# Optimization experiments

Measured on AMD Instinct MI355X. Metric: run time of the kernel, lower is better.

Reference implementation:

```python
import jax, jax.numpy as jnp
import numpy as np


def setup_inputs() -> dict:
    key = jax.random.key(0)
    k1, k2 = jax.random.split(key)
    B, T, D, E = 4, 4096, 2048, 64
    x = jax.random.normal(k1, (B, T, D), dtype=jnp.float32)
    gate_w = jax.random.normal(k2, (E, D), dtype=jnp.float32) * (1.0 / np.sqrt(D))
    return {"x": x, "gate_w": gate_w, "top_k": 2}


def reference(x, gate_w, top_k):
    B, T, D = x.shape
    x_flat = x.reshape(-1, D)                      # (B*T, D)
    logits = jnp.einsum('nd,ed->ne', x_flat, gate_w)  # (B*T, E)
    weights, indices = jax.lax.top_k(logits, top_k)   # (B*T, K)
    weights = jax.nn.softmax(weights, axis=-1)
    return indices, weights
```

## Files before the change

### kernel.cpp

```cpp
#include <hip/hip_runtime.h>
#include <hip/hip_bf16.h>
#include <math.h>


constexpr int D_DIM = 2048;
constexpr int E_DIM = 64;
constexpr int BM    = 32;
constexpr int BKC   = 64;
constexpr int NCH   = D_DIM / BKC;
constexpr int CHF   = BM * BKC / 2 + BKC * E_DIM / 2;
constexpr int LPAD  = 68;

typedef __attribute__((ext_vector_type(8))) short s16x8;
typedef __attribute__((ext_vector_type(4))) float f32x4;

static __device__ __forceinline__ short f2bf(float f) {
    __hip_bfloat16 h = __float2bfloat16(f);
    return *reinterpret_cast<short*>(&h);
}
static __device__ __forceinline__ float b2f(short s) {
    union { unsigned u; float f; } x;
    x.u = ((unsigned)(unsigned short)s) << 16;
    return x.f;
}

__global__ __launch_bounds__(256, 1)
void pack_w(const float* __restrict__ w, short* __restrict__ wsb) {
    const int idx = blockIdx.x * 256 + threadIdx.x;
    const int e = idx >> 11, k = idx & 2047;
    const float v = w[idx];
    const short hi = f2bf(v);
    const short lo = f2bf(v - b2f(hi));
    const int g = k >> 3, j = k & 7;
    const size_t base = (size_t)g * 1024 + e * 8 + j;
    wsb[base]       = hi;
    wsb[base + 512] = lo;
}

template <bool PACKED>
__global__ __launch_bounds__(512, 4)
void router_v7(const float* __restrict__ x,
               const float* __restrict__ w,
               const short* __restrict__ wsb,
               float* __restrict__ out,
               int nrows) {
    __shared__ alignas(16) float smem[2][6144];

    const int t    = threadIdx.x;
    const int lane = t & 63;
    const int wv   = t >> 6;
    const int row0 = blockIdx.x * BM;
    const int l15  = lane & 15;
    const int k8   = lane >> 4;
    const int rsel = wv & 1;
    const int e0w  = (wv >> 1) * 16;
    const int ph   = blockIdx.x & (NCH - 1);

    auto stage = [&](int b, int cc) {
        #pragma unroll
        for (int q = 0; q < 3; ++q) {
            const int i = wv * 3 + q;
            const char* src;
            if (i < 8) {
                const int r = 4 * i + (lane >> 4);
                src = (const char*)x + (size_t)(row0 + r) * (D_DIM * 4)
                    + cc * 256 + (((lane & 15) * 16) ^ ((r & 7) << 4));
            } else {
                const int j = i - 8;
                if (PACKED)
                    src = (const char*)wsb + (size_t)cc * 16384 + j * 1024 + lane * 16;
                else {
                    const int gl = j >> 1;
                    const int e  = (j & 1) * 32 + (lane >> 1);
                    src = (const char*)w + (size_t)e * (D_DIM * 4)
                        + (cc * BKC + gl * 8) * 4 + (lane & 1) * 16;
                }
            }
            __builtin_amdgcn_global_load_lds(
                (const __attribute__((address_space(1))) void*)src,
                (__attribute__((address_space(3))) void*)((char*)&smem[b][0] + i * 1024),
                16, 0, 0);
        }
    };

    f32x4 acc;
    #pragma unroll
    for (int j = 0; j < 4; ++j) acc[j] = 0.f;

    auto compute = [&](int b) {
        const char* Ab = (const char*)&smem[b][0];
        const char* Bb = Ab + 8192;
        const int r    = 16 * rsel + l15;
        const int swz  = (r & 7) << 4;
        #pragma unroll
        for (int s = 0; s < 2; ++s) {
            const int gl  = s * 4 + k8;
            const char* rp = Ab + r * 256;
            const int off  = s * 128 + k8 * 32;
            const float4 v0 = *reinterpret_cast<const float4*>(rp + (off ^ swz));
            const float4 v1 = *reinterpret_cast<const float4*>(rp + ((off + 16) ^ swz));
            const float vv[8] = {v0.x, v0.y, v0.z, v0.w, v1.x, v1.y, v1.z, v1.w};
            s16x8 ah, al;
            #pragma unroll
            for (int j = 0; j < 8; ++j) {
                const short h = f2bf(vv[j]);
                ah[j] = h;
                al[j] = f2bf(vv[j] - b2f(h));
            }
            s16x8 bh, bl;
            if (PACKED) {
                const char* bp = Bb + gl * 2048 + (e0w + l15) * 16;
                bh = *reinterpret_cast<const s16x8*>(bp);
                bl = *reinterpret_cast<const s16x8*>(bp + 1024);
            } else {
                const char* bp = Bb + ((size_t)gl * 64 + e0w + l15) * 32;
                const float4 w0 = *reinterpret_cast<const float4*>(bp);
                const float4 w1 = *reinterpret_cast<const float4*>(bp + 16);
                const float wvv[8] = {w0.x, w0.y, w0.z, w0.w, w1.x, w1.y, w1.z, w1.w};
                #pragma unroll
                for (int j = 0; j < 8; ++j) {
                    const short h = f2bf(wvv[j]);
                    bh[j] = h;
                    bl[j] = f2bf(wvv[j] - b2f(h));
                }
            }
            acc = __builtin_amdgcn_mfma_f32_16x16x32_bf16(al, bh, acc, 0, 0, 0);
            acc = __builtin_amdgcn_mfma_f32_16x16x32_bf16(ah, bl, acc, 0, 0, 0);
            acc = __builtin_amdgcn_mfma_f32_16x16x32_bf16(ah, bh, acc, 0, 0, 0);
        }
    };

    stage(0, ph);
    stage(1, (ph + 1) & (NCH - 1));
    #pragma unroll 1
    for (int c = 0; c < NCH; ++c) {
        if (c + 1 < NCH) asm volatile("s_waitcnt vmcnt(3)" ::: "memory");
        else             asm volatile("s_waitcnt vmcnt(0)" ::: "memory");
        __builtin_amdgcn_s_barrier();
        asm volatile("" ::: "memory");
        compute(c & 1);
        asm volatile("s_waitcnt lgkmcnt(0)" ::: "memory");
        __builtin_amdgcn_s_barrier();
        asm volatile("" ::: "memory");
        if (c + 2 < NCH) stage(c & 1, (c + 2 + ph) & (NCH - 1));
    }

    float* lgs = &smem[0][0];
    #pragma unroll
    for (int j = 0; j < 4; ++j)
        lgs[(16 * rsel + k8 * 4 + j) * LPAD + e0w + l15] = acc[j];
    __syncthreads();

    if (wv < 4) {
        const int row = wv * 8 + (lane >> 3);
        const int seg = lane & 7;
        const float* rp = &lgs[row * LPAD + seg * 8];
        const float4 a  = *reinterpret_cast<const float4*>(rp);
        const float4 bq = *reinterpret_cast<const float4*>(rp + 4);
        const float sv[8] = {a.x, a.y, a.z, a.w, bq.x, bq.y, bq.z, bq.w};
        float m1 = sv[0]; int i1 = seg * 8;
        float m2 = -INFINITY; int i2 = 0;
        #pragma unroll
        for (int j = 1; j < 8; ++j) {
            const float v = sv[j]; const int idx = seg * 8 + j;
            if (v > m1)      { m2 = m1; i2 = i1; m1 = v; i1 = idx; }
            else if (v > m2) { m2 = v;  i2 = idx; }
        }
        #pragma unroll
        for (int d = 1; d < 8; d <<= 1) {
            const float M1 = __shfl_xor(m1, d); const int I1 = __shfl_xor(i1, d);
            const float M2 = __shfl_xor(m2, d); const int I2 = __shfl_xor(i2, d);
            const bool sw = (M1 > m1) || (M1 == m1 && I1 < i1);
            const float a1 = sw ? M1 : m1; const int j1 = sw ? I1 : i1;
            const float b1 = sw ? m1 : M1; const int kx = sw ? i1 : I1;
            const float a2 = sw ? M2 : m2; const int j2 = sw ? I2 : i2;
            const bool t2 = (b1 > a2) || (b1 == a2 && kx < j2);
            m1 = a1; i1 = j1;
            m2 = t2 ? b1 : a2; i2 = t2 ? kx : j2;
        }
        if (seg == 0) {
            const float e2v = expf(m2 - m1);
            const float sm  = 1.0f + e2v;
            const long  r   = row0 + row;
            const long  off = (long)nrows * 2;
            out[2 * r + 0]       = (float)i1;
            out[2 * r + 1]       = (float)i2;
            out[off + 2 * r + 0] = 1.0f / sm;
            out[off + 2 * r + 1] = e2v / sm;
        }
    }
}

extern "C" void kernel_launch(void* const* d_in, const int* in_sizes, int n_in,
                              void* d_out, int out_size, void* d_ws, size_t ws_size,
                              hipStream_t stream) {
    const float* x = (const float*)d_in[0];
    const float* w = (const float*)d_in[1];
    float* out = (float*)d_out;
    short* wsb = (short*)d_ws;
    const int nrows = in_sizes[0] / D_DIM;
    const int grid  = nrows / BM;
    const bool packed = ws_size >= (size_t)(E_DIM * D_DIM) * 2 * sizeof(short);

    if (packed) {
        hipLaunchKernelGGL(pack_w, dim3(E_DIM * D_DIM / 256), dim3(256), 0, stream, w, wsb);
        hipLaunchKernelGGL(router_v7<true>, dim3(grid), dim3(512), 0, stream,
                           x, w, wsb, out, nrows);
    } else {
        hipLaunchKernelGGL(router_v7<false>, dim3(grid), dim3(512), 0, stream,
                           x, w, wsb, out, nrows);
    }
}
```

Measured before the change: 42.19 us.

## Load gate weights straight to registers and deepen x staging to four buffers

The weight operand now goes from global memory (the packed workspace) straight into per-wave registers instead of being staged through LDS. The x tile is still staged in LDS with async global_load_lds, but the pipeline is now four chunks deep instead of two, with vmcnt waits counted per stage. The aim is to keep more of the memory-bound x stream in flight and to cut LDS use per block. In exchange, the B fragments use more registers, and waves that share expert columns now each fetch weight data from cache on their own.

```diff
diff --git a/kernel.cpp b/kernel.cpp
--- a/kernel.cpp
+++ b/kernel.cpp
@@ -8,7 +8,6 @@
 constexpr int BM    = 32;
 constexpr int BKC   = 64;
 constexpr int NCH   = D_DIM / BKC;
-constexpr int CHF   = BM * BKC / 2 + BKC * E_DIM / 2;
 constexpr int LPAD  = 68;
 
 typedef __attribute__((ext_vector_type(8))) short s16x8;
@@ -22,6 +21,10 @@
     union { unsigned u; float f; } x;
     x.u = ((unsigned)(unsigned short)s) << 16;
     return x.f;
+}
+
+template <int N> static __device__ __forceinline__ void waitvm() {
+    asm volatile("s_waitcnt vmcnt(%0)" :: "n"(N) : "memory");
 }
 
 __global__ __launch_bounds__(256, 1)
@@ -39,12 +42,12 @@
 
 template <bool PACKED>
 __global__ __launch_bounds__(512, 4)
-void router_v7(const float* __restrict__ x,
+void router_v8(const float* __restrict__ x,
                const float* __restrict__ w,
                const short* __restrict__ wsb,
                float* __restrict__ out,
                int nrows) {
-    __shared__ alignas(16) float smem[2][6144];
+    __shared__ alignas(16) float smem[4][BM * BKC / 4 * 4];
 
     const int t    = threadIdx.x;
     const int lane = t & 63;
@@ -55,48 +58,59 @@
     const int rsel = wv & 1;
     const int e0w  = (wv >> 1) * 16;
     const int ph   = blockIdx.x & (NCH - 1);
-
-    auto stage = [&](int b, int cc) {
-        #pragma unroll
-        for (int q = 0; q < 3; ++q) {
-            const int i = wv * 3 + q;
-            const char* src;
-            if (i < 8) {
-                const int r = 4 * i + (lane >> 4);
-                src = (const char*)x + (size_t)(row0 + r) * (D_DIM * 4)
-                    + cc * 256 + (((lane & 15) * 16) ^ ((r & 7) << 4));
-            } else {
-                const int j = i - 8;
-                if (PACKED)
-                    src = (const char*)wsb + (size_t)cc * 16384 + j * 1024 + lane * 16;
-                else {
-                    const int gl = j >> 1;
-                    const int e  = (j & 1) * 32 + (lane >> 1);
-                    src = (const char*)w + (size_t)e * (D_DIM * 4)
-                        + (cc * BKC + gl * 8) * 4 + (lane & 1) * 16;
+    const char* wsb_b = (const char*)wsb;
+
+    s16x8 Bh[4][2], Bl[4][2];
+
+    auto loadB = [&](int p, int c) {
+        const int cc = (c + ph) & (NCH - 1);
+        if constexpr (PACKED) {
+            #pragma unroll
+            for (int s = 0; s < 2; ++s) {
+                const char* bp = wsb_b + (size_t)cc * 16384
+                               + (s * 4 + k8) * 2048 + (e0w + l15) * 16;
+                Bh[p][s] = *reinterpret_cast<const s16x8*>(bp);
+                Bl[p][s] = *reinterpret_cast<const s16x8*>(bp + 1024);
+            }
+        } else {
+            #pragma unroll
+            for (int s = 0; s < 2; ++s) {
+                const float* pw = w + (size_t)(e0w + l15) * D_DIM
+                                + cc * BKC + (s * 4 + k8) * 8;
+                const float4 w0 = *reinterpret_cast<const float4*>(pw);
+                const float4 w1 = *reinterpret_cast<const float4*>(pw + 4);
+                const float wvv[8] = {w0.x, w0.y, w0.z, w0.w, w1.x, w1.y, w1.z, w1.w};
+                #pragma unroll
+                for (int j = 0; j < 8; ++j) {
+                    const short h = f2bf(wvv[j]);
+                    Bh[p][s][j] = h;
+                    Bl[p][s][j] = f2bf(wvv[j] - b2f(h));
                 }
             }
-            __builtin_amdgcn_global_load_lds(
-                (const __attribute__((address_space(1))) void*)src,
-                (__attribute__((address_space(3))) void*)((char*)&smem[b][0] + i * 1024),
-                16, 0, 0);
-        }
+        }
+    };
+
+    auto stageA = [&](int p, int c) {
+        const int cc = (c + ph) & (NCH - 1);
+        const int r  = 4 * wv + (lane >> 4);
+        const char* src = (const char*)x + (size_t)(row0 + r) * (D_DIM * 4)
+                        + cc * 256 + ((l15 * 16) ^ ((r & 7) << 4));
+        __builtin_amdgcn_global_load_lds(
+            (const __attribute__((address_space(1))) void*)src,
+            (__attribute__((address_space(3))) void*)((char*)&smem[p][0] + wv * 1024),
+            16, 0, 0);
     };
 
     f32x4 acc;
     #pragma unroll
     for (int j = 0; j < 4; ++j) acc[j] = 0.f;
 
-    auto compute = [&](int b) {
-        const char* Ab = (const char*)&smem[b][0];
-        const char* Bb = Ab + 8192;
-        const int r    = 16 * rsel + l15;
-        const int swz  = (r & 7) << 4;
+    auto compute = [&](int p) {
+        const char* rp  = (const char*)&smem[p][0] + (16 * rsel + l15) * 256;
+        const int   swz = ((16 * rsel + l15) & 7) << 4;
         #pragma unroll
         for (int s = 0; s < 2; ++s) {
-            const int gl  = s * 4 + k8;
-            const char* rp = Ab + r * 256;
-            const int off  = s * 128 + k8 * 32;
+            const int off = s * 128 + k8 * 32;
             const float4 v0 = *reinterpret_cast<const float4*>(rp + (off ^ swz));
             const float4 v1 = *reinterpret_cast<const float4*>(rp + ((off + 16) ^ swz));
             const float vv[8] = {v0.x, v0.y, v0.z, v0.w, v1.x, v1.y, v1.z, v1.w};
@@ -107,43 +121,36 @@
                 ah[j] = h;
                 al[j] = f2bf(vv[j] - b2f(h));
             }
-            s16x8 bh, bl;
-            if (PACKED) {
-                const char* bp = Bb + gl * 2048 + (e0w + l15) * 16;
-                bh = *reinterpret_cast<const s16x8*>(bp);
-                bl = *reinterpret_cast<const s16x8*>(bp + 1024);
-            } else {
-                const char* bp = Bb + ((size_t)gl * 64 + e0w + l15) * 32;
-                const float4 w0 = *reinterpret_cast<const float4*>(bp);
-                const float4 w1 = *reinterpret_cast<const float4*>(bp + 16);
-                const float wvv[8] = {w0.x, w0.y, w0.z, w0.w, w1.x, w1.y, w1.z, w1.w};
-                #pragma unroll
-                for (int j = 0; j < 8; ++j) {
-                    const short h = f2bf(wvv[j]);
-                    bh[j] = h;
-                    bl[j] = f2bf(wvv[j] - b2f(h));
-                }
-            }
-            acc = __builtin_amdgcn_mfma_f32_16x16x32_bf16(al, bh, acc, 0, 0, 0);
-            acc = __builtin_amdgcn_mfma_f32_16x16x32_bf16(ah, bl, acc, 0, 0, 0);
-            acc = __builtin_amdgcn_mfma_f32_16x16x32_bf16(ah, bh, acc, 0, 0, 0);
+            acc = __builtin_amdgcn_mfma_f32_16x16x32_bf16(al, Bh[p][s], acc, 0, 0, 0);
+            acc = __builtin_amdgcn_mfma_f32_16x16x32_bf16(ah, Bl[p][s], acc, 0, 0, 0);
+            acc = __builtin_amdgcn_mfma_f32_16x16x32_bf16(ah, Bh[p][s], acc, 0, 0, 0);
         }
     };
 
-    stage(0, ph);
-    stage(1, (ph + 1) & (NCH - 1));
+    #pragma unroll
+    for (int p = 0; p < 4; ++p) { loadB(p, p); stageA(p, p); }
+
     #pragma unroll 1
-    for (int c = 0; c < NCH; ++c) {
-        if (c + 1 < NCH) asm volatile("s_waitcnt vmcnt(3)" ::: "memory");
-        else             asm volatile("s_waitcnt vmcnt(0)" ::: "memory");
-        __builtin_amdgcn_s_barrier();
-        asm volatile("" ::: "memory");
-        compute(c & 1);
-        asm volatile("s_waitcnt lgkmcnt(0)" ::: "memory");
-        __builtin_amdgcn_s_barrier();
-        asm volatile("" ::: "memory");
-        if (c + 2 < NCH) stage(c & 1, (c + 2 + ph) & (NCH - 1));
+    for (int cq = 0; cq < 7; ++cq) {
+        #pragma unroll
+        for (int p = 0; p < 4; ++p) {
+            waitvm<15>();
+            __builtin_amdgcn_s_barrier();
+            asm volatile("" ::: "memory");
+            compute(p);
+            asm volatile("s_waitcnt lgkmcnt(0)" ::: "memory");
+            __builtin_amdgcn_s_barrier();
+            asm volatile("" ::: "memory");
+            const int c = cq * 4 + p + 4;
+            loadB(p, c);
+            stageA(p, c);
+        }
     }
+    waitvm<15>(); __builtin_amdgcn_s_barrier(); asm volatile("" ::: "memory"); compute(0);
+    waitvm<10>(); __builtin_amdgcn_s_barrier(); asm volatile("" ::: "memory"); compute(1);
+    waitvm<5>();  __builtin_amdgcn_s_barrier(); asm volatile("" ::: "memory"); compute(2);
+    waitvm<0>();  __builtin_amdgcn_s_barrier(); asm volatile("" ::: "memory"); compute(3);
+    __syncthreads();
 
     float* lgs = &smem[0][0];
     #pragma unroll
@@ -204,10 +211,10 @@
 
     if (packed) {
         hipLaunchKernelGGL(pack_w, dim3(E_DIM * D_DIM / 256), dim3(256), 0, stream, w, wsb);
-        hipLaunchKernelGGL(router_v7<true>, dim3(grid), dim3(512), 0, stream,
+        hipLaunchKernelGGL(router_v8<true>, dim3(grid), dim3(512), 0, stream,
                            x, w, wsb, out, nrows);
     } else {
-        hipLaunchKernelGGL(router_v7<false>, dim3(grid), dim3(512), 0, stream,
+        hipLaunchKernelGGL(router_v8<false>, dim3(grid), dim3(512), 0, stream,
                            x, w, wsb, out, nrows);
     }
 }
```

Result: faster. 41.05 us (-2.7%).
